# Kernel tuning notes

Hardware: AMD Instinct MI355X
Metric: run time of the kernel (lower is better)

Reference implementation:

```python
import jax, jax.numpy as jnp
import numpy as np

K = 16                 # hardcoded k in KL_divergence default
TYPICAL_CRLB = 0.15 * 100 / 10   # = 1.5, sigma used in KL divergence


def setup_inputs() -> dict:
    key = jax.random.key(0)
    k1, k2 = jax.random.split(key)
    N = 8192
    ch1 = jax.random.normal(k1, (N, 2), dtype=jnp.float32)
    ch2 = jax.random.normal(k2, (N, 2), dtype=jnp.float32)
    # Polynomial layer parameters, exactly as in __init__ (identity-ish map)
    M1 = jnp.array([[0.0, 0.0], [1.0, 0.0]], dtype=jnp.float32)
    M2 = jnp.array([[0.0, 1.0], [0.0, 0.0]], dtype=jnp.float32)
    return {"ch1": ch1, "ch2": ch2, "M1": M1, "M2": M2}


def _polynomial(x, M1, M2):
    # out[:,0] = sum_ij M1[i,j] * x1^i * x2^j ; out[:,1] analog with M2 (m=2)
    x1, x2 = x[:, 0], x[:, 1]
    pi = jnp.stack([jnp.ones_like(x1), x1], axis=1)          # [N,2] -> x1^i
    pj = jnp.stack([jnp.ones_like(x2), x2], axis=1)          # [N,2] -> x2^j
    B = pi[:, :, None] * pj[:, None, :]                      # [N,2,2] basis x1^i*x2^j
    y1 = jnp.einsum('nij,ij->n', B, M1)
    y2 = jnp.einsum('nij,ij->n', B, M2)
    return jnp.stack([y1, y2], axis=1)                       # [N,2]


def reference(ch1, ch2, M1, M2):
    N = ch1.shape[0]
    ch2m = _polynomial(ch2, M1, M2)

    # --- KNN ---
    diff = ch1[None, :, :] - ch2m[:, None, :]                # [N2, N1, 2]
    distances = diff * diff                                  # squared per-coord dists
    abs_distances = jnp.sum(distances, axis=2)               # [N2, N1]
    # top_k of negated transposed distances: for each ch1 point, k nearest ch2m
    _, idx = jax.lax.top_k(-abs_distances.T, K)              # [N1, K] indices into ch2 axis
    # Faithful reproduction of the original index construction:
    # idx is flattened row-major ([N,K]); indx1 flattens a [K,N] arange-broadcast,
    # so the second coordinate at flat position t is t % N.
    flat_a = idx.reshape(-1)                                 # [N*K] indexes axis 0 (ch2)
    flat_b = jnp.tile(jnp.arange(N), K)                      # [N*K] indexes axis 1 (ch1)
    knn = distances[flat_a, flat_b].reshape(K, N, 2)         # [K, N, 2]

    # --- KL divergence ---
    sigma2 = TYPICAL_CRLB
    D_KL = 0.5 * jnp.sum(knn / (sigma2 ** 2), axis=2)        # [K, N]

    # --- Rel entropy ---
    expD = jnp.sum(jnp.exp(-D_KL), axis=0) / N               # [N]
    mask = expD != 0.0                                       # tf boolean_mask of nonzeros
    safe = jnp.where(mask, expD, 1.0)
    return -jnp.sum(jnp.where(mask, jnp.log(safe), 0.0))
```

## Files before the change

### kernel.cpp

```cpp
#include <hip/hip_runtime.h>
#include <math.h>
#include <stdint.h>

#define K_NN 16
#define NPTS 8192
#define NR 32
#define PADN (NPTS + 64)

static __device__ __constant__ float d_bt[33] = {
    -3.4028235e38f,
    -1.8627318f, -1.5341205f, -1.3180109f, -1.1503494f, -1.0100762f,
    -0.8871466f, -0.7764218f, -0.6744898f, -0.5791322f, -0.4887764f,
    -0.4022501f, -0.3186394f, -0.2372021f, -0.1573107f, -0.0784124f,
     0.0f,
     0.0784124f,  0.1573107f,  0.2372021f,  0.3186394f,  0.4022501f,
     0.4887764f,  0.5791322f,  0.6744898f,  0.7764218f,  0.8871466f,
     1.0100762f,  1.1503494f,  1.3180109f,  1.5341205f,  1.8627318f,
     3.4028235e38f
};

__device__ __forceinline__ int rowOf(const float* bt, float y) {
    int c = 0;
    c += (y >= bt[c + 16]) ? 16 : 0;
    c += (y >= bt[c + 8])  ? 8  : 0;
    c += (y >= bt[c + 4])  ? 4  : 0;
    c += (y >= bt[c + 2])  ? 2  : 0;
    c += (y >= bt[c + 1])  ? 1  : 0;
    return c;
}

__global__ __launch_bounds__(1024) void kb_build(const float* __restrict__ ch2,
                                                 const float* __restrict__ M1,
                                                 const float* __restrict__ M2,
                                                 float2* __restrict__ spts,
                                                 int* __restrict__ rowStart,
                                                 float* __restrict__ out) {
    __shared__ float2 lsp[PADN];
    __shared__ int h[NR];
    __shared__ int offs[NR];
    __shared__ float bt[33];
    const int tid = threadIdx.x;
    if (tid == 0) out[0] = 0.0f;
    if (tid < 33) bt[tid] = d_bt[tid];
    if (tid < NR) h[tid] = 0;
    const float inf = __int_as_float(0x7F800000);
    for (int i = tid; i < PADN; i += 1024) lsp[i] = make_float2(inf, inf);
    __syncthreads();

    const float a0 = M1[0], a1 = M1[1], a2 = M1[2], a3 = M1[3];
    const float b0 = M2[0], b1 = M2[1], b2 = M2[2], b3 = M2[3];
    const float4* __restrict__ g4 = (const float4*)ch2;

    float2 pts[8];
    int rw[8];
#pragma unroll
    for (int e = 0; e < 4; ++e) {
        float4 v = g4[e * 1024 + tid];
        pts[2 * e]     = make_float2(a0 + a1 * v.y + v.x * (a2 + a3 * v.y),
                                     b0 + b1 * v.y + v.x * (b2 + b3 * v.y));
        pts[2 * e + 1] = make_float2(a0 + a1 * v.w + v.z * (a2 + a3 * v.w),
                                     b0 + b1 * v.w + v.z * (b2 + b3 * v.w));
    }
#pragma unroll
    for (int p = 0; p < 8; ++p) {
        rw[p] = rowOf(bt, pts[p].y);
        atomicAdd(&h[rw[p]], 1);
    }
    __syncthreads();

    if (tid == 0) {
        int run = 0;
        for (int r = 0; r < NR; ++r) {
            offs[r] = run;
            rowStart[r] = run;
            run += (h[r] + 1) & ~1;
        }
        rowStart[NR] = run;
    }
    __syncthreads();

#pragma unroll
    for (int p = 0; p < 8; ++p) {
        int gi = 2 * ((p >> 1) * 1024 + tid) + (p & 1);
        int pos = atomicAdd(&offs[rw[p]], 1);
        unsigned ux = (__float_as_uint(pts[p].x) & ~0x7Fu) | ((unsigned)gi >> 6);
        unsigned uy = (__float_as_uint(pts[p].y) & ~0x3Fu) | ((unsigned)gi & 63u);
        lsp[pos] = make_float2(__uint_as_float(ux), __uint_as_float(uy));
    }
    __syncthreads();

    for (int i = tid; i < PADN / 2; i += 1024)
        ((float4*)spts)[i] = ((float4*)lsp)[i];
}

__global__ __launch_bounds__(1024) void kq_query(const float* __restrict__ ch1,
                                                 const float2* __restrict__ spts,
                                                 const int* __restrict__ rowStart,
                                                 int* __restrict__ midx) {
    __shared__ float2 shp[PADN];
    const int tid  = threadIdx.x;
    const int lane = tid & 63;
    const int w    = tid >> 6;
    const int qg   = blockIdx.x * 16 + w;

    for (int i = tid; i < PADN / 2; i += 1024)
        ((float4*)shp)[i] = ((const float4*)spts)[i];

    int rsv = rowStart[lane < 33 ? lane : 0];
    int btb = __float_as_int(d_bt[lane < 33 ? lane : 0]);
    __syncthreads();

    const float qx = ch1[2 * qg + 0];
    const float qy = ch1[2 * qg + 1];
    const int own = rowOf(d_bt, qy);

    unsigned key = 0xFFFFFFFFu;
    unsigned thr = 0xFFFFFFFFu;
    bool first = true;

#define SCAN_ROW(R)                                                            \
    {                                                                          \
        int lo = __builtin_amdgcn_readlane(rsv, (R));                          \
        int hi = __builtin_amdgcn_readlane(rsv, (R) + 1);       \
        for (int base = lo; base < hi; base += 128) {                          \
            int i0 = base + 2 * lane;                                          \
            int ii = min(i0, hi - 2);                         \
            float4 cc = *(const float4*)&shp[ii];                              \
            bool a0 = i0 < hi;                                                 \
            bool a1 = i0 + 1 < hi;                                             \
            float dx0 = qx - cc.x, dy0 = qy - cc.y;                            \
            float dx1 = qx - cc.z, dy1 = qy - cc.w;                            \
            unsigned u0 = a0 ? __float_as_uint(dx0 * dx0 + dy0 * dy0)          \
                             : 0xFFFFFFFFu;                                    \
            unsigned u1 = a1 ? __float_as_uint(dx1 * dx1 + dy1 * dy1)          \
                             : 0xFFFFFFFFu;                                    \
            if (first) {                                                       \
                first = false;                                                 \
                unsigned mn = min(u0, u1);                                     \
                mn = min(mn, (unsigned)__shfl_xor((int)mn, 1, 64));            \
                mn = min(mn, (unsigned)__shfl_xor((int)mn, 2, 64));            \
                unsigned mx = mn;                                              \
                mx = max(mx, (unsigned)__shfl_xor((int)mx, 4, 64));            \
                mx = max(mx, (unsigned)__shfl_xor((int)mx, 8, 64));            \
                mx = max(mx, (unsigned)__shfl_xor((int)mx, 16, 64));           \
                mx = max(mx, (unsigned)__shfl_xor((int)mx, 32, 64));           \
                thr = mx | 0x1FFFu;                                            \
            }                                                                  \
            unsigned id0 = ((__float_as_uint(cc.x) & 0x7Fu) << 6)              \
                         | (__float_as_uint(cc.y) & 0x3Fu);                    \
            unsigned id1 = ((__float_as_uint(cc.z) & 0x7Fu) << 6)              \
                         | (__float_as_uint(cc.w) & 0x3Fu);                    \
            unsigned nk0 = (u0 & 0xFFFFE000u) | id0;                           \
            unsigned nk1 = (u1 & 0xFFFFE000u) | id1;                           \
            unsigned long long m0 = __ballot(u0 <= thr);                       \
            unsigned long long m1 = __ballot(u1 <= thr);                       \
            while (m0) {                                                       \
                int l = __ffsll(m0) - 1;                                       \
                m0 &= m0 - 1;                                                  \
                unsigned snk = (unsigned)__builtin_amdgcn_readlane((int)nk0, l);\
                unsigned up = (unsigned)__builtin_amdgcn_update_dpp(           \
                    0, (int)key, 0x111, 0xF, 0xF, false);       \
                bool c1 = snk < key;                                           \
                unsigned nv = (snk < up) ? up : snk;                           \
                key = c1 ? nv : key;                                           \
            }                                                                  \
            while (m1) {                                                       \
                int l = __ffsll(m1) - 1;                                       \
                m1 &= m1 - 1;                                                  \
                unsigned snk = (unsigned)__builtin_amdgcn_readlane((int)nk1, l);\
                unsigned up = (unsigned)__builtin_amdgcn_update_dpp(           \
                    0, (int)key, 0x111, 0xF, 0xF, false);                      \
                bool c1 = snk < key;                                           \
                unsigned nv = (snk < up) ? up : snk;                           \
                key = c1 ? nv : key;                                           \
            }                                                                  \
            thr = (unsigned)__builtin_amdgcn_readlane((int)key, 15) | 0x1FFFu; \
        }                                                                      \
    }

    SCAN_ROW(own)

    bool loDone = false, hiDone = false;
    for (int d = 1; d < NR; ++d) {
        int rlo = own - d, rhi = own + d;
        if (!loDone) {
            if (rlo < 0) loDone = true;
            else {
                float band = qy - __uint_as_float(
                    __builtin_amdgcn_readlane(btb, rlo + 1));
                unsigned bb = __float_as_uint(band * band) & 0xFFFFE000u;
                if (bb > (thr & 0xFFFFE000u)) loDone = true;
                else SCAN_ROW(rlo)
            }
        }
        if (!hiDone) {
            if (rhi > NR - 1) hiDone = true;
            else {
                float band = __uint_as_float(
                    __builtin_amdgcn_readlane(btb, rhi)) - qy;
                unsigned bb = __float_as_uint(band * band) & 0xFFFFE000u;
                if (bb > (thr & 0xFFFFE000u)) hiDone = true;
                else SCAN_ROW(rhi)
            }
        }
        if (loDone && hiDone) break;
    }
#undef SCAN_ROW

    if (lane < K_NN)
        midx[qg * K_NN + lane] = (int)(key & 0x1FFFu);
}

__global__ __launch_bounds__(1024) void k3_final(const float* __restrict__ ch1,
                                                 const float* __restrict__ ch2,
                                                 const float* __restrict__ M1,
                                                 const float* __restrict__ M2,
                                                 const int* __restrict__ midx,
                                                 float* __restrict__ out, int N) {
    const float a0 = M1[0], a1 = M1[1], a2 = M1[2], a3 = M1[3];
    const float b0 = M2[0], b1 = M2[1], b2 = M2[2], b3 = M2[3];

    int t = blockIdx.x * 1024 + threadIdx.x;
    int n = t >> 4;
    int k = t & 15;
    int g = n >> 4;
    int r = n & 15;

    int j = k * (N / K_NN) + g;
    int a = midx[j * K_NN + r];
    float2 cp = ((const float2*)ch2)[a];
    float cx = a0 + a1 * cp.y + cp.x * (a2 + a3 * cp.y);
    float cy = b0 + b1 * cp.y + cp.x * (b2 + b3 * cp.y);
    float dx = ch1[2 * n + 0] - cx;
    float dy = ch1[2 * n + 1] - cy;
    float term = expf(-(dx * dx + dy * dy) * (1.0f / 4.5f));

#pragma unroll
    for (int off = 8; off; off >>= 1) term += __shfl_down(term, off, 16);

    float v = 0.0f;
    if (k == 0) {
        float expD = term / (float)N;
        v = (expD != 0.0f) ? logf(expD) : 0.0f;
    }
#pragma unroll
    for (int off = 32; off; off >>= 1) v += __shfl_down(v, off, 64);

    __shared__ float red[16];
    int lane = threadIdx.x & 63;
    int wv = threadIdx.x >> 6;
    if (lane == 0) red[wv] = v;
    __syncthreads();
    if (threadIdx.x == 0) {
        float s = 0.0f;
#pragma unroll
        for (int i = 0; i < 16; ++i) s += red[i];
        atomicAdd(out, -s);
    }
}

extern "C" void kernel_launch(void* const* d_in, const int* in_sizes, int n_in,
                              void* d_out, int out_size, void* d_ws, size_t ws_size,
                              hipStream_t stream) {
    const float* ch1 = (const float*)d_in[0];
    const float* ch2 = (const float*)d_in[1];
    const float* M1  = (const float*)d_in[2];
    const float* M2  = (const float*)d_in[3];
    float* out = (float*)d_out;
    const int N = in_sizes[0] / 2;

    char* ws = (char*)d_ws;
    float2* spts     = (float2*)ws;
    int*    rowStart = (int*)(ws + 66560);
    int*    midx     = (int*)(ws + 66560 + 256);

    kb_build<<<1, 1024, 0, stream>>>(ch2, M1, M2, spts, rowStart, out);

    kq_query<<<N / 16, 1024, 0, stream>>>(ch1, spts, rowStart, midx);

    k3_final<<<(N * K_NN) / 1024, 1024, 0, stream>>>(ch1, ch2, M1, M2, midx, out, N);
}
```

Baseline: 89.82 us.

## Fuse grid build into query kernel, rebuilding sorted points per block

Removes the single-block build kernel and has every query block bin and sort the transformed ch2 points into shared memory itself. This drops one kernel launch, the serial one-block stage and the workspace round trip. In exchange, each of the 512 blocks redundantly reads ch2, runs shared-memory atomics and scatters the points before it starts querying.

New measurement: 87.89 us. 1.02x faster.

```diff
diff --git a/kernel.cpp b/kernel.cpp
--- a/kernel.cpp
+++ b/kernel.cpp
@@ -29,22 +29,29 @@
     return c;
 }
 
-__global__ __launch_bounds__(1024) void kb_build(const float* __restrict__ ch2,
+__global__ __launch_bounds__(1024) void kq_fused(const float* __restrict__ ch1,
+                                                 const float* __restrict__ ch2,
                                                  const float* __restrict__ M1,
                                                  const float* __restrict__ M2,
-                                                 float2* __restrict__ spts,
-                                                 int* __restrict__ rowStart,
+                                                 int* __restrict__ midx,
                                                  float* __restrict__ out) {
-    __shared__ float2 lsp[PADN];
+    __shared__ __align__(16) float2 shp[PADN];
     __shared__ int h[NR];
     __shared__ int offs[NR];
+    __shared__ int rs[NR + 1];
     __shared__ float bt[33];
-    const int tid = threadIdx.x;
-    if (tid == 0) out[0] = 0.0f;
+
+    const int tid  = threadIdx.x;
+    const int lane = tid & 63;
+    const int w    = tid >> 6;
+    const int qg   = blockIdx.x * 16 + w;
+
+    if (blockIdx.x == 0 && tid == 0) out[0] = 0.0f;
+
     if (tid < 33) bt[tid] = d_bt[tid];
     if (tid < NR) h[tid] = 0;
     const float inf = __int_as_float(0x7F800000);
-    for (int i = tid; i < PADN; i += 1024) lsp[i] = make_float2(inf, inf);
+    for (int i = tid; i < PADN; i += 1024) shp[i] = make_float2(inf, inf);
     __syncthreads();
 
     const float a0 = M1[0], a1 = M1[1], a2 = M1[2], a3 = M1[3];
@@ -72,10 +79,10 @@
         int run = 0;
         for (int r = 0; r < NR; ++r) {
             offs[r] = run;
-            rowStart[r] = run;
+            rs[r] = run;
             run += (h[r] + 1) & ~1;
         }
-        rowStart[NR] = run;
+        rs[NR] = run;
     }
     __syncthreads();
 
@@ -85,30 +92,12 @@
         int pos = atomicAdd(&offs[rw[p]], 1);
         unsigned ux = (__float_as_uint(pts[p].x) & ~0x7Fu) | ((unsigned)gi >> 6);
         unsigned uy = (__float_as_uint(pts[p].y) & ~0x3Fu) | ((unsigned)gi & 63u);
-        lsp[pos] = make_float2(__uint_as_float(ux), __uint_as_float(uy));
-    }
-    __syncthreads();
-
-    for (int i = tid; i < PADN / 2; i += 1024)
-        ((float4*)spts)[i] = ((float4*)lsp)[i];
-}
-
-__global__ __launch_bounds__(1024) void kq_query(const float* __restrict__ ch1,
-                                                 const float2* __restrict__ spts,
-                                                 const int* __restrict__ rowStart,
-                                                 int* __restrict__ midx) {
-    __shared__ float2 shp[PADN];
-    const int tid  = threadIdx.x;
-    const int lane = tid & 63;
-    const int w    = tid >> 6;
-    const int qg   = blockIdx.x * 16 + w;
-
-    for (int i = tid; i < PADN / 2; i += 1024)
-        ((float4*)shp)[i] = ((const float4*)spts)[i];
-
-    int rsv = rowStart[lane < 33 ? lane : 0];
+        shp[pos] = make_float2(__uint_as_float(ux), __uint_as_float(uy));
+    }
+    __syncthreads();
+
+    int rsv = rs[lane < 33 ? lane : 0];
     int btb = __float_as_int(d_bt[lane < 33 ? lane : 0]);
-    __syncthreads();
 
     const float qx = ch1[2 * qg + 0];
     const float qy = ch1[2 * qg + 1];
@@ -126,13 +115,13 @@
             int i0 = base + 2 * lane;                                          \
             int ii = min(i0, hi - 2);                         \
             float4 cc = *(const float4*)&shp[ii];                              \
-            bool a0 = i0 < hi;                                                 \
-            bool a1 = i0 + 1 < hi;                                             \
+            bool p0 = i0 < hi;                                                 \
+            bool p1 = i0 + 1 < hi;                                             \
             float dx0 = qx - cc.x, dy0 = qy - cc.y;                            \
             float dx1 = qx - cc.z, dy1 = qy - cc.w;                            \
-            unsigned u0 = a0 ? __float_as_uint(dx0 * dx0 + dy0 * dy0)          \
+            unsigned u0 = p0 ? __float_as_uint(dx0 * dx0 + dy0 * dy0)          \
                              : 0xFFFFFFFFu;                                    \
-            unsigned u1 = a1 ? __float_as_uint(dx1 * dx1 + dy1 * dy1)          \
+            unsigned u1 = p1 ? __float_as_uint(dx1 * dx1 + dy1 * dy1)          \
                              : 0xFFFFFFFFu;                                    \
             if (first) {                                                       \
                 first = false;                                                 \
@@ -269,14 +258,9 @@
     float* out = (float*)d_out;
     const int N = in_sizes[0] / 2;
 
-    char* ws = (char*)d_ws;
-    float2* spts     = (float2*)ws;
-    int*    rowStart = (int*)(ws + 66560);
-    int*    midx     = (int*)(ws + 66560 + 256);
-
-    kb_build<<<1, 1024, 0, stream>>>(ch2, M1, M2, spts, rowStart, out);
-
-    kq_query<<<N / 16, 1024, 0, stream>>>(ch1, spts, rowStart, midx);
+    int* midx = (int*)d_ws;
+
+    kq_fused<<<N / 16, 1024, 0, stream>>>(ch1, ch2, M1, M2, midx, out);
 
     k3_final<<<(N * K_NN) / 1024, 1024, 0, stream>>>(ch1, ch2, M1, M2, midx, out, N);
 }
```
